# Kernel tuning notes

Measured on AMD Instinct MI355X. Metric: run time of the kernel, lower is better.

## Reference

```python
import jax, jax.numpy as jnp
import numpy as np

BULK, TOWER, E8D = 2048, 512, 8
NUM_LEVELS = 8  # training_levels
LN_EPS = 1e-6
RMS_EPS = 1e-6


def _layernorm(x, g, b, eps=LN_EPS):
    mu = jnp.mean(x, axis=-1, keepdims=True)
    var = jnp.mean((x - mu) ** 2, axis=-1, keepdims=True)
    return (x - mu) * jax.lax.rsqrt(var + eps) * g + b


def _rmsnorm(x, scale, eps=RMS_EPS):
    rms = jnp.sqrt(jnp.mean(x ** 2, axis=-1, keepdims=True) + eps)
    return x / rms * scale


def _nearest_d8(x):
    # Nearest point in D8 (integer vectors with even coordinate sum).
    f = jnp.round(x)
    err = x - f
    parity_odd = jnp.mod(jnp.sum(f, axis=-1), 2.0) != 0
    idx = jnp.argmax(jnp.abs(err), axis=-1)
    oh = jax.nn.one_hot(idx, E8D, dtype=x.dtype)
    worst_err = jnp.take_along_axis(err, idx[..., None], axis=-1)
    adj = jnp.where(worst_err >= 0, 1.0, -1.0)
    f_fix = f + oh * adj  # flip rounding of worst coordinate to restore even parity
    return jnp.where(parity_odd[..., None], f_fix, f)


def _nearest_e8(x):
    # E8 = D8 U (D8 + 1/2); pick the closer candidate.
    a = _nearest_d8(x)
    b = _nearest_d8(x - 0.5) + 0.5
    da = jnp.sum((x - a) ** 2, axis=-1)
    db = jnp.sum((x - b) ** 2, axis=-1)
    return jnp.where((da <= db)[..., None], a, b)


def _residual_e8_quantize(x, num_levels=NUM_LEVELS):
    # Residual VQ: per-level nearest E8 lattice point, subtract, accumulate.
    r = x
    q = jnp.zeros_like(x)
    for _ in range(num_levels):
        ql = _nearest_e8(r)
        q = q + ql
        r = r - ql
    return q


def setup_inputs() -> dict:
    key = jax.random.key(0)
    ks = jax.random.split(key, 8)
    B, S = 8, 2048
    s_bt = 1.0 / np.sqrt(BULK)
    s_t = 1.0 / np.sqrt(TOWER)
    s_e = 1.0 / np.sqrt(E8D)
    return {
        'x': jax.random.normal(ks[0], (B, S, BULK), dtype=jnp.float32),
        'W_bt': jax.random.uniform(ks[1], (BULK, TOWER), jnp.float32, -s_bt, s_bt),
        'b_bt': jnp.zeros((TOWER,), jnp.float32),
        'ln_et_g': jnp.ones((TOWER,), jnp.float32),
        'ln_et_b': jnp.zeros((TOWER,), jnp.float32),
        'W_t8': jax.random.uniform(ks[2], (TOWER, E8D), jnp.float32, -s_t, s_t),
        'b_t8': jnp.zeros((E8D,), jnp.float32),
        'rms_g': jnp.ones((E8D,), jnp.float32),
        'W_8t': jax.random.uniform(ks[3], (E8D, TOWER), jnp.float32, -s_e, s_e),
        'b_8t': jnp.zeros((TOWER,), jnp.float32),
        'ln_dt_g': jnp.ones((TOWER,), jnp.float32),
        'ln_dt_b': jnp.zeros((TOWER,), jnp.float32),
        'W_tb': jax.random.uniform(ks[4], (TOWER, BULK), jnp.float32, -s_t, s_t),
        'b_tb': jnp.zeros((BULK,), jnp.float32),
        'ln_db_g': jnp.ones((BULK,), jnp.float32),
        'ln_db_b': jnp.zeros((BULK,), jnp.float32),
    }


def reference(x, W_bt, b_bt, ln_et_g, ln_et_b, W_t8, b_t8, rms_g,
              W_8t, b_8t, ln_dt_g, ln_dt_b, W_tb, b_tb, ln_db_g, ln_db_b):
    B, S, D = x.shape
    h = x.reshape(B * S, D)
    # encode: bulk -> tower -> 8D continuous
    tower = _layernorm(h @ W_bt + b_bt, ln_et_g, ln_et_b)
    e8 = _rmsnorm(tower @ W_t8 + b_t8, rms_g)
    # residual E8 lattice quantization with straight-through estimator
    q = _residual_e8_quantize(e8, NUM_LEVELS)
    e8_q = e8 + jax.lax.stop_gradient(q - e8)
    # decode: 8D -> tower -> bulk
    t2 = _layernorm(e8_q @ W_8t + b_8t, ln_dt_g, ln_dt_b)
    out = _layernorm(t2 @ W_tb + b_tb, ln_db_g, ln_db_b)
    return out.reshape(B, S, D)
```

## Files before the change

### kernel.cpp

```cpp
#include <hip/hip_runtime.h>

#define BULK 2048
#define TOWER 512
#define E8D 8
#define NROWS 16384
#define LO_SCALE 2048.0f
#define LO_INV (1.0f / 2048.0f)

typedef _Float16 f16x8 __attribute__((ext_vector_type(8)));
typedef float f32x4 __attribute__((ext_vector_type(4)));

#define GLOAD(g, l)                                                        \
    __builtin_amdgcn_global_load_lds(                                      \
        (const __attribute__((address_space(1))) void*)(g),                \
        (__attribute__((address_space(3))) void*)(l), 16, 0, 0)

__global__ void k_conv_transpose(const float* __restrict__ in, int K, int N,
                                 _Float16* __restrict__ out_hi,
                                 _Float16* __restrict__ out_lo) {
    __shared__ float tile[32][33];
    int tx = threadIdx.x & 31, ty = threadIdx.x >> 5;
    int k0 = blockIdx.x * 32, n0 = blockIdx.y * 32;
#pragma unroll
    for (int i = 0; i < 32; i += 8)
        tile[ty + i][tx] = in[(size_t)(k0 + ty + i) * N + (n0 + tx)];
    __syncthreads();
#pragma unroll
    for (int i = 0; i < 32; i += 8) {
        int n = n0 + ty + i, k = k0 + tx;
        float v = tile[tx][ty + i];
        _Float16 h = (_Float16)v;
        _Float16 l = (_Float16)((v - (float)h) * LO_SCALE);
        out_hi[(size_t)n * K + k] = h;
        out_lo[(size_t)n * K + k] = l;
    }
}

template <bool A_FP32>
__global__ __launch_bounds__(256, 2) void k_gemm_split(
    const float* __restrict__ Af, const _Float16* __restrict__ Ah,
    const _Float16* __restrict__ Al, const _Float16* __restrict__ Bh,
    const _Float16* __restrict__ Bl, float* __restrict__ C, int K, int N) {
    __shared__ _Float16 lds[2][4][128][32];
    const int t = threadIdx.x;
    const int m0 = blockIdx.x * 128, n0 = blockIdx.y * 128;
    const int wid = t >> 6, lane = t & 63;
    const int wr = wid >> 1, wc = wid & 1;
    const int lr = lane & 15, kg = lane >> 4;

    f32x4 acc1[4][4] = {};
    f32x4 acc2[4][4] = {};

    const int sr = t >> 1, sc = (t & 1) * 16;
    const float* aptr = A_FP32 ? (Af + (size_t)(m0 + sr) * K + sc) : nullptr;
    float areg[16];

    const int c0 = wid * 2;
    const _Float16* bhp =
        Bh + (size_t)(n0 + c0 * 16 + (lane >> 2)) * K + (lane & 3) * 8;
    const _Float16* blp =
        Bl + (size_t)(n0 + c0 * 16 + (lane >> 2)) * K + (lane & 3) * 8;

    const _Float16* gop = (wid == 0) ? Ah : (wid == 1) ? Al : (wid == 2) ? Bh : Bl;
    const int r0 = ((wid < 2) ? m0 : n0) + (lane >> 2);
    const _Float16* gp = A_FP32 ? nullptr : (gop + (size_t)r0 * K + (lane & 3) * 8);

    auto loadA = [&](int k0) {
        const float* p = aptr + k0;
        *(float4*)&areg[0] = *(const float4*)(p);
        *(float4*)&areg[4] = *(const float4*)(p + 4);
        *(float4*)&areg[8] = *(const float4*)(p + 8);
        *(float4*)&areg[12] = *(const float4*)(p + 12);
    };
    auto stageB = [&](int k0, int bb) {
        GLOAD(bhp + k0, &lds[bb][2][c0 * 16][0]);
        GLOAD(bhp + k0 + (size_t)16 * K, &lds[bb][2][c0 * 16 + 16][0]);
        GLOAD(blp + k0, &lds[bb][3][c0 * 16][0]);
        GLOAD(blp + k0 + (size_t)16 * K, &lds[bb][3][c0 * 16 + 16][0]);
    };
    auto writeA = [&](int bb) {
        f16x8 hv0, hv1, lv0, lv1;
#pragma unroll
        for (int e = 0; e < 8; ++e) {
            float va = areg[e], vb = areg[8 + e];
            _Float16 ha = (_Float16)va, hb = (_Float16)vb;
            hv0[e] = ha;
            hv1[e] = hb;
            lv0[e] = (_Float16)((va - (float)ha) * LO_SCALE);
            lv1[e] = (_Float16)((vb - (float)hb) * LO_SCALE);
        }
        *(f16x8*)&lds[bb][0][sr][sc] = hv0;
        *(f16x8*)&lds[bb][0][sr][sc + 8] = hv1;
        *(f16x8*)&lds[bb][1][sr][sc] = lv0;
        *(f16x8*)&lds[bb][1][sr][sc + 8] = lv1;
    };
    auto stageAll = [&](int k0, int bb) {
#pragma unroll
        for (int j = 0; j < 8; ++j)
            GLOAD(gp + k0 + (size_t)(j * 16) * K, &lds[bb][wid][j * 16][0]);
    };

    if constexpr (A_FP32) {
        loadA(0);
        stageB(0, 0);
        writeA(0);
    } else {
        stageAll(0, 0);
    }
    __syncthreads();

    const int nk = K / 32;
    for (int kt = 0; kt < nk; ++kt) {
        const int b = kt & 1;
        if (kt + 1 < nk) {
            if constexpr (A_FP32) {
                loadA((kt + 1) * 32);
                stageB((kt + 1) * 32, b ^ 1);
            } else {
                stageAll((kt + 1) * 32, b ^ 1);
            }
        }

        f16x8 a_h[4], a_l[4], b_h[4], b_l[4];
#pragma unroll
        for (int m = 0; m < 4; ++m) {
            int r = wr * 64 + m * 16 + lr;
            a_h[m] = *(const f16x8*)&lds[b][0][r][kg * 8];
            a_l[m] = *(const f16x8*)&lds[b][1][r][kg * 8];
        }
#pragma unroll
        for (int n = 0; n < 4; ++n) {
            int r = wc * 64 + n * 16 + lr;
            b_h[n] = *(const f16x8*)&lds[b][2][r][kg * 8];
            b_l[n] = *(const f16x8*)&lds[b][3][r][kg * 8];
        }
#pragma unroll
        for (int m = 0; m < 4; ++m)
#pragma unroll
            for (int n = 0; n < 4; ++n) {
                acc1[m][n] = __builtin_amdgcn_mfma_f32_16x16x32_f16(
                    a_h[m], b_h[n], acc1[m][n], 0, 0, 0);
                acc2[m][n] = __builtin_amdgcn_mfma_f32_16x16x32_f16(
                    a_h[m], b_l[n], acc2[m][n], 0, 0, 0);
                acc2[m][n] = __builtin_amdgcn_mfma_f32_16x16x32_f16(
                    a_l[m], b_h[n], acc2[m][n], 0, 0, 0);
            }

        if constexpr (A_FP32) {
            if (kt + 1 < nk) writeA(b ^ 1);
        }
        __syncthreads();
    }

#pragma unroll
    for (int m = 0; m < 4; ++m)
#pragma unroll
        for (int n = 0; n < 4; ++n)
#pragma unroll
            for (int i = 0; i < 4; ++i) {
                int row = m0 + wr * 64 + m * 16 + kg * 4 + i;
                int col = n0 + wc * 64 + n * 16 + lr;
                C[(size_t)row * N + col] = acc1[m][n][i] + acc2[m][n][i] * LO_INV;
            }
}

__device__ inline void nearest_d8(const float* x, float* f) {
    float s = 0.f;
#pragma unroll
    for (int j = 0; j < 8; ++j) {
        f[j] = rintf(x[j]);
        s += f[j];
    }
    float besta = -1.f, beste = 0.f;
    int bidx = 0;
#pragma unroll
    for (int j = 0; j < 8; ++j) {
        float e = x[j] - f[j];
        float a = fabsf(e);
        if (a > besta) { besta = a; beste = e; bidx = j; }
    }
    if (fmodf(s, 2.0f) != 0.0f) {
        float adj = (beste >= 0.f) ? 1.f : -1.f;
#pragma unroll
        for (int j = 0; j < 8; ++j) f[j] += (j == bidx) ? adj : 0.f;
    }
}

__device__ inline void nearest_e8(const float* x, float* out) {
    float fa[8], xs[8], fb[8];
    nearest_d8(x, fa);
#pragma unroll
    for (int j = 0; j < 8; ++j) xs[j] = x[j] - 0.5f;
    nearest_d8(xs, fb);
#pragma unroll
    for (int j = 0; j < 8; ++j) fb[j] += 0.5f;
    float da = 0.f, db = 0.f;
#pragma unroll
    for (int j = 0; j < 8; ++j) {
        float ea = x[j] - fa[j], eb = x[j] - fb[j];
        da += ea * ea;
        db += eb * eb;
    }
    bool pa = (da <= db);
#pragma unroll
    for (int j = 0; j < 8; ++j) out[j] = pa ? fa[j] : fb[j];
}

__device__ inline float wred64(float v) {
#pragma unroll
    for (int off = 1; off < 64; off <<= 1) v += __shfl_xor(v, off, 64);
    return v;
}

__global__ __launch_bounds__(256) void k_rows(
    const float* __restrict__ pre1, const float* __restrict__ b_bt,
    const float* __restrict__ g_et, const float* __restrict__ be_et,
    const float* __restrict__ W_t8, const float* __restrict__ b_t8,
    const float* __restrict__ rms_g, const float* __restrict__ W_8t,
    const float* __restrict__ b_8t, const float* __restrict__ g_dt,
    const float* __restrict__ b_dt, _Float16* __restrict__ t2h,
    _Float16* __restrict__ t2l) {
    int wid = threadIdx.x >> 6, lane = threadIdx.x & 63;
    int row = blockIdx.x * 4 + wid;
    int cb = lane * 8;

    const float* src = pre1 + (size_t)row * TOWER + cb;
    float v[8];
    *(float4*)&v[0] = *(const float4*)(src);
    *(float4*)&v[4] = *(const float4*)(src + 4);
#pragma unroll
    for (int i = 0; i < 8; ++i) v[i] += b_bt[cb + i];

    float s = 0.f;
#pragma unroll
    for (int i = 0; i < 8; ++i) s += v[i];
    s = wred64(s);
    float mu = s * (1.f / 512.f);
    float ss = 0.f;
#pragma unroll
    for (int i = 0; i < 8; ++i) { float d = v[i] - mu; ss += d * d; }
    ss = wred64(ss);
    float inv = 1.f / sqrtf(ss * (1.f / 512.f) + 1e-6f);
    float tw[8];
#pragma unroll
    for (int i = 0; i < 8; ++i)
        tw[i] = (v[i] - mu) * inv * g_et[cb + i] + be_et[cb + i];

    float p[8] = {0.f, 0.f, 0.f, 0.f, 0.f, 0.f, 0.f, 0.f};
#pragma unroll
    for (int i = 0; i < 8; ++i) {
        const float* wr_ = W_t8 + (size_t)(cb + i) * 8;
#pragma unroll
        for (int j = 0; j < 8; ++j) p[j] += tw[i] * wr_[j];
    }
#pragma unroll
    for (int j = 0; j < 8; ++j) p[j] = wred64(p[j]);

    float e8[8];
    float ms = 0.f;
#pragma unroll
    for (int j = 0; j < 8; ++j) {
        e8[j] = p[j] + b_t8[j];
        ms += e8[j] * e8[j];
    }
    float rms = sqrtf(ms * (1.f / 8.f) + 1e-6f);
#pragma unroll
    for (int j = 0; j < 8; ++j) e8[j] = e8[j] / rms * rms_g[j];

    float q[8] = {0.f, 0.f, 0.f, 0.f, 0.f, 0.f, 0.f, 0.f};
    float r[8];
#pragma unroll
    for (int j = 0; j < 8; ++j) r[j] = e8[j];
#pragma unroll
    for (int lvl = 0; lvl < 8; ++lvl) {
        float ql[8];
        nearest_e8(r, ql);
#pragma unroll
        for (int j = 0; j < 8; ++j) { q[j] += ql[j]; r[j] -= ql[j]; }
    }

    float o[8];
#pragma unroll
    for (int i = 0; i < 8; ++i) {
        int c = cb + i;
        float acc = b_8t[c];
#pragma unroll
        for (int j = 0; j < 8; ++j) acc += q[j] * W_8t[(size_t)j * TOWER + c];
        o[i] = acc;
    }
    float s2 = 0.f;
#pragma unroll
    for (int i = 0; i < 8; ++i) s2 += o[i];
    s2 = wred64(s2);
    float mu2 = s2 * (1.f / 512.f);
    float ss2 = 0.f;
#pragma unroll
    for (int i = 0; i < 8; ++i) { float d = o[i] - mu2; ss2 += d * d; }
    ss2 = wred64(ss2);
    float inv2 = 1.f / sqrtf(ss2 * (1.f / 512.f) + 1e-6f);

    f16x8 hv, lv;
#pragma unroll
    for (int i = 0; i < 8; ++i) {
        int c = cb + i;
        float t2v = (o[i] - mu2) * inv2 * g_dt[c] + b_dt[c];
        _Float16 h = (_Float16)t2v;
        hv[i] = h;
        lv[i] = (_Float16)((t2v - (float)h) * LO_SCALE);
    }
    *(f16x8*)(t2h + (size_t)row * TOWER + cb) = hv;
    *(f16x8*)(t2l + (size_t)row * TOWER + cb) = lv;
}

__global__ __launch_bounds__(256) void k_ln2(float* __restrict__ out,
                                             const float* __restrict__ b_tb,
                                             const float* __restrict__ g,
                                             const float* __restrict__ b) {
    __shared__ float red[4];
    int t = threadIdx.x, wid = t >> 6, lane = t & 63;
    size_t base = (size_t)blockIdx.x * BULK;
    int cb = t * 8;
    float v[8];
    *(float4*)&v[0] = *(const float4*)(out + base + cb);
    *(float4*)&v[4] = *(const float4*)(out + base + cb + 4);
#pragma unroll
    for (int i = 0; i < 8; ++i) v[i] += b_tb[cb + i];

    float s = 0.f;
#pragma unroll
    for (int i = 0; i < 8; ++i) s += v[i];
    s = wred64(s);
    if (lane == 0) red[wid] = s;
    __syncthreads();
    float tot = red[0] + red[1] + red[2] + red[3];
    float mu = tot * (1.f / 2048.f);
    __syncthreads();
    float ss = 0.f;
#pragma unroll
    for (int i = 0; i < 8; ++i) { float d = v[i] - mu; ss += d * d; }
    ss = wred64(ss);
    if (lane == 0) red[wid] = ss;
    __syncthreads();
    float vtot = red[0] + red[1] + red[2] + red[3];
    float inv = 1.f / sqrtf(vtot * (1.f / 2048.f) + 1e-6f);
#pragma unroll
    for (int i = 0; i < 8; ++i) v[i] = (v[i] - mu) * inv * g[cb + i] + b[cb + i];
    *(float4*)(out + base + cb) = *(float4*)&v[0];
    *(float4*)(out + base + cb + 4) = *(float4*)&v[4];
}

extern "C" void kernel_launch(void* const* d_in, const int* in_sizes, int n_in,
                              void* d_out, int out_size, void* d_ws,
                              size_t ws_size, hipStream_t stream) {
    const float* x     = (const float*)d_in[0];
    const float* W_bt  = (const float*)d_in[1];
    const float* b_bt  = (const float*)d_in[2];
    const float* g_et  = (const float*)d_in[3];
    const float* be_et = (const float*)d_in[4];
    const float* W_t8  = (const float*)d_in[5];
    const float* b_t8  = (const float*)d_in[6];
    const float* rms_g = (const float*)d_in[7];
    const float* W_8t  = (const float*)d_in[8];
    const float* b_8t  = (const float*)d_in[9];
    const float* g_dt  = (const float*)d_in[10];
    const float* b_dt  = (const float*)d_in[11];
    const float* W_tb  = (const float*)d_in[12];
    const float* b_tb  = (const float*)d_in[13];
    const float* g_db  = (const float*)d_in[14];
    const float* b_db  = (const float*)d_in[15];
    float* out = (float*)d_out;

    char* w = (char*)d_ws;
    _Float16* Wbt_h = (_Float16*)w; w += (size_t)BULK * TOWER * 2;
    _Float16* Wbt_l = (_Float16*)w; w += (size_t)BULK * TOWER * 2;
    _Float16* Wtb_h = (_Float16*)w; w += (size_t)TOWER * BULK * 2;
    _Float16* Wtb_l = (_Float16*)w; w += (size_t)TOWER * BULK * 2;
    _Float16* t2h   = (_Float16*)w; w += (size_t)NROWS * TOWER * 2;
    _Float16* t2l   = (_Float16*)w; w += (size_t)NROWS * TOWER * 2;
    float* pre1 = out;

    k_conv_transpose<<<dim3(BULK / 32, TOWER / 32), 256, 0, stream>>>(
        W_bt, BULK, TOWER, Wbt_h, Wbt_l);
    k_conv_transpose<<<dim3(TOWER / 32, BULK / 32), 256, 0, stream>>>(
        W_tb, TOWER, BULK, Wtb_h, Wtb_l);

    k_gemm_split<true><<<dim3(NROWS / 128, TOWER / 128), 256, 0, stream>>>(
        x, nullptr, nullptr, Wbt_h, Wbt_l, pre1, BULK, TOWER);

    k_rows<<<NROWS / 4, 256, 0, stream>>>(pre1, b_bt, g_et, be_et, W_t8, b_t8,
                                          rms_g, W_8t, b_8t, g_dt, b_dt, t2h,
                                          t2l);

    k_gemm_split<false><<<dim3(NROWS / 128, BULK / 128), 256, 0, stream>>>(
        nullptr, t2h, t2l, Wtb_h, Wtb_l, out, TOWER, BULK);

    k_ln2<<<NROWS, 256, 0, stream>>>(out, b_tb, g_db, b_db);
}
```

Before: 545.0 us.

## Drop split-fp16 low part in decode GEMM and split quantization into separate kernel

The second GEMM (tower->bulk) now uses plain fp16 operands with a single MFMA per tile instead of the three-MFMA hi/lo split, which halves its LDS traffic and cuts its matrix work by about two thirds. The residual E8 quantization, which previously ran redundantly on all 64 lanes of each wave, is moved into its own kernel that runs one thread per row. Extra launches and small intermediate buffers are added. Precision of the decode projection drops to fp16 inputs, which the final layernorm may or may not tolerate.

```diff
diff --git a/kernel.cpp b/kernel.cpp
--- a/kernel.cpp
+++ b/kernel.cpp
@@ -15,6 +15,7 @@
         (const __attribute__((address_space(1))) void*)(g),                \
         (__attribute__((address_space(3))) void*)(l), 16, 0, 0)
 
+template <bool LO>
 __global__ void k_conv_transpose(const float* __restrict__ in, int K, int N,
                                  _Float16* __restrict__ out_hi,
                                  _Float16* __restrict__ out_lo) {
@@ -30,18 +31,19 @@
         int n = n0 + ty + i, k = k0 + tx;
         float v = tile[tx][ty + i];
         _Float16 h = (_Float16)v;
-        _Float16 l = (_Float16)((v - (float)h) * LO_SCALE);
         out_hi[(size_t)n * K + k] = h;
-        out_lo[(size_t)n * K + k] = l;
-    }
-}
-
-template <bool A_FP32>
+        if constexpr (LO)
+            out_lo[(size_t)n * K + k] = (_Float16)((v - (float)h) * LO_SCALE);
+    }
+}
+
+template <int MODE>
 __global__ __launch_bounds__(256, 2) void k_gemm_split(
     const float* __restrict__ Af, const _Float16* __restrict__ Ah,
-    const _Float16* __restrict__ Al, const _Float16* __restrict__ Bh,
-    const _Float16* __restrict__ Bl, float* __restrict__ C, int K, int N) {
-    __shared__ _Float16 lds[2][4][128][32];
+    const _Float16* __restrict__ Bh, const _Float16* __restrict__ Bl,
+    float* __restrict__ C, int K, int N) {
+    constexpr int NOPS = (MODE == 0) ? 4 : 2;
+    __shared__ _Float16 lds[2][NOPS][128][32];
     const int t = threadIdx.x;
     const int m0 = blockIdx.x * 128, n0 = blockIdx.y * 128;
     const int wid = t >> 6, lane = t & 63;
@@ -52,18 +54,20 @@
     f32x4 acc2[4][4] = {};
 
     const int sr = t >> 1, sc = (t & 1) * 16;
-    const float* aptr = A_FP32 ? (Af + (size_t)(m0 + sr) * K + sc) : nullptr;
+    const float* aptr = nullptr;
+    const _Float16 *bhp = nullptr, *blp = nullptr, *gp = nullptr;
     float areg[16];
-
     const int c0 = wid * 2;
-    const _Float16* bhp =
-        Bh + (size_t)(n0 + c0 * 16 + (lane >> 2)) * K + (lane & 3) * 8;
-    const _Float16* blp =
-        Bl + (size_t)(n0 + c0 * 16 + (lane >> 2)) * K + (lane & 3) * 8;
-
-    const _Float16* gop = (wid == 0) ? Ah : (wid == 1) ? Al : (wid == 2) ? Bh : Bl;
-    const int r0 = ((wid < 2) ? m0 : n0) + (lane >> 2);
-    const _Float16* gp = A_FP32 ? nullptr : (gop + (size_t)r0 * K + (lane & 3) * 8);
+
+    if constexpr (MODE == 0) {
+        aptr = Af + (size_t)(m0 + sr) * K + sc;
+        bhp = Bh + (size_t)(n0 + c0 * 16 + (lane >> 2)) * K + (lane & 3) * 8;
+        blp = Bl + (size_t)(n0 + c0 * 16 + (lane >> 2)) * K + (lane & 3) * 8;
+    } else {
+        const _Float16* gop = (wid >> 1) ? Bh : Ah;
+        const int r0 = ((wid >> 1) ? n0 : m0) + (wid & 1) * 64 + (lane >> 2);
+        gp = gop + (size_t)r0 * K + (lane & 3) * 8;
+    }
 
     auto loadA = [&](int k0) {
         const float* p = aptr + k0;
@@ -96,11 +100,12 @@
     };
     auto stageAll = [&](int k0, int bb) {
 #pragma unroll
-        for (int j = 0; j < 8; ++j)
-            GLOAD(gp + k0 + (size_t)(j * 16) * K, &lds[bb][wid][j * 16][0]);
+        for (int j = 0; j < 4; ++j)
+            GLOAD(gp + k0 + (size_t)(j * 16) * K,
+                  &lds[bb][wid >> 1][(wid & 1) * 64 + j * 16][0]);
     };
 
-    if constexpr (A_FP32) {
+    if constexpr (MODE == 0) {
         loadA(0);
         stageB(0, 0);
         writeA(0);
@@ -113,7 +118,7 @@
     for (int kt = 0; kt < nk; ++kt) {
         const int b = kt & 1;
         if (kt + 1 < nk) {
-            if constexpr (A_FP32) {
+            if constexpr (MODE == 0) {
                 loadA((kt + 1) * 32);
                 stageB((kt + 1) * 32, b ^ 1);
             } else {
@@ -121,33 +126,50 @@
             }
         }
 
-        f16x8 a_h[4], a_l[4], b_h[4], b_l[4];
-#pragma unroll
-        for (int m = 0; m < 4; ++m) {
-            int r = wr * 64 + m * 16 + lr;
-            a_h[m] = *(const f16x8*)&lds[b][0][r][kg * 8];
-            a_l[m] = *(const f16x8*)&lds[b][1][r][kg * 8];
-        }
-#pragma unroll
-        for (int n = 0; n < 4; ++n) {
-            int r = wc * 64 + n * 16 + lr;
-            b_h[n] = *(const f16x8*)&lds[b][2][r][kg * 8];
-            b_l[n] = *(const f16x8*)&lds[b][3][r][kg * 8];
-        }
-#pragma unroll
-        for (int m = 0; m < 4; ++m)
+        if constexpr (MODE == 0) {
+            f16x8 a_h[4], a_l[4], b_h[4], b_l[4];
+#pragma unroll
+            for (int m = 0; m < 4; ++m) {
+                int r = wr * 64 + m * 16 + lr;
+                a_h[m] = *(const f16x8*)&lds[b][0][r][kg * 8];
+                a_l[m] = *(const f16x8*)&lds[b][1][r][kg * 8];
+            }
 #pragma unroll
             for (int n = 0; n < 4; ++n) {
-                acc1[m][n] = __builtin_amdgcn_mfma_f32_16x16x32_f16(
-                    a_h[m], b_h[n], acc1[m][n], 0, 0, 0);
-                acc2[m][n] = __builtin_amdgcn_mfma_f32_16x16x32_f16(
-                    a_h[m], b_l[n], acc2[m][n], 0, 0, 0);
-                acc2[m][n] = __builtin_amdgcn_mfma_f32_16x16x32_f16(
-                    a_l[m], b_h[n], acc2[m][n], 0, 0, 0);
-            }
-
-        if constexpr (A_FP32) {
+                int r = wc * 64 + n * 16 + lr;
+                b_h[n] = *(const f16x8*)&lds[b][2][r][kg * 8];
+                b_l[n] = *(const f16x8*)&lds[b][3][r][kg * 8];
+            }
+#pragma unroll
+            for (int m = 0; m < 4; ++m)
+#pragma unroll
+                for (int n = 0; n < 4; ++n) {
+                    acc1[m][n] = __builtin_amdgcn_mfma_f32_16x16x32_f16(
+                        a_h[m], b_h[n], acc1[m][n], 0, 0, 0);
+                    acc2[m][n] = __builtin_amdgcn_mfma_f32_16x16x32_f16(
+                        a_h[m], b_l[n], acc2[m][n], 0, 0, 0);
+                    acc2[m][n] = __builtin_amdgcn_mfma_f32_16x16x32_f16(
+                        a_l[m], b_h[n], acc2[m][n], 0, 0, 0);
+                }
             if (kt + 1 < nk) writeA(b ^ 1);
+        } else {
+            f16x8 a_h[4], b_h[4];
+#pragma unroll
+            for (int m = 0; m < 4; ++m) {
+                int r = wr * 64 + m * 16 + lr;
+                a_h[m] = *(const f16x8*)&lds[b][0][r][kg * 8];
+            }
+#pragma unroll
+            for (int n = 0; n < 4; ++n) {
+                int r = wc * 64 + n * 16 + lr;
+                b_h[n] = *(const f16x8*)&lds[b][1][r][kg * 8];
+            }
+#pragma unroll
+            for (int m = 0; m < 4; ++m)
+#pragma unroll
+                for (int n = 0; n < 4; ++n)
+                    acc1[m][n] = __builtin_amdgcn_mfma_f32_16x16x32_f16(
+                        a_h[m], b_h[n], acc1[m][n], 0, 0, 0);
         }
         __syncthreads();
     }
@@ -160,7 +182,9 @@
             for (int i = 0; i < 4; ++i) {
                 int row = m0 + wr * 64 + m * 16 + kg * 4 + i;
                 int col = n0 + wc * 64 + n * 16 + lr;
-                C[(size_t)row * N + col] = acc1[m][n][i] + acc2[m][n][i] * LO_INV;
+                float v = acc1[m][n][i];
+                if constexpr (MODE == 0) v += acc2[m][n][i] * LO_INV;
+                C[(size_t)row * N + col] = v;
             }
 }
 
@@ -212,14 +236,11 @@
     return v;
 }
 
-__global__ __launch_bounds__(256) void k_rows(
+__global__ __launch_bounds__(256) void k_rows_a(
     const float* __restrict__ pre1, const float* __restrict__ b_bt,
     const float* __restrict__ g_et, const float* __restrict__ be_et,
     const float* __restrict__ W_t8, const float* __restrict__ b_t8,
-    const float* __restrict__ rms_g, const float* __restrict__ W_8t,
-    const float* __restrict__ b_8t, const float* __restrict__ g_dt,
-    const float* __restrict__ b_dt, _Float16* __restrict__ t2h,
-    _Float16* __restrict__ t2l) {
+    const float* __restrict__ rms_g, float* __restrict__ e8buf) {
     int wid = threadIdx.x >> 6, lane = threadIdx.x & 63;
     int row = blockIdx.x * 4 + wid;
     int cb = lane * 8;
@@ -267,10 +288,21 @@
 #pragma unroll
     for (int j = 0; j < 8; ++j) e8[j] = e8[j] / rms * rms_g[j];
 
+    if (lane == 0) {
+        float4 f0 = {e8[0], e8[1], e8[2], e8[3]};
+        float4 f1 = {e8[4], e8[5], e8[6], e8[7]};
+        *(float4*)(e8buf + (size_t)row * 8) = f0;
+        *(float4*)(e8buf + (size_t)row * 8 + 4) = f1;
+    }
+}
+
+__global__ __launch_bounds__(256) void k_quant(const float* __restrict__ e8buf,
+                                               float* __restrict__ qbuf) {
+    int row = blockIdx.x * 256 + threadIdx.x;
+    float r[8];
+    *(float4*)&r[0] = *(const float4*)(e8buf + (size_t)row * 8);
+    *(float4*)&r[4] = *(const float4*)(e8buf + (size_t)row * 8 + 4);
     float q[8] = {0.f, 0.f, 0.f, 0.f, 0.f, 0.f, 0.f, 0.f};
-    float r[8];
-#pragma unroll
-    for (int j = 0; j < 8; ++j) r[j] = e8[j];
 #pragma unroll
     for (int lvl = 0; lvl < 8; ++lvl) {
         float ql[8];
@@ -278,6 +310,23 @@
 #pragma unroll
         for (int j = 0; j < 8; ++j) { q[j] += ql[j]; r[j] -= ql[j]; }
     }
+    float4 f0 = {q[0], q[1], q[2], q[3]};
+    float4 f1 = {q[4], q[5], q[6], q[7]};
+    *(float4*)(qbuf + (size_t)row * 8) = f0;
+    *(float4*)(qbuf + (size_t)row * 8 + 4) = f1;
+}
+
+__global__ __launch_bounds__(256) void k_rows_b(
+    const float* __restrict__ qbuf, const float* __restrict__ W_8t,
+    const float* __restrict__ b_8t, const float* __restrict__ g_dt,
+    const float* __restrict__ b_dt, _Float16* __restrict__ t2h) {
+    int wid = threadIdx.x >> 6, lane = threadIdx.x & 63;
+    int row = blockIdx.x * 4 + wid;
+    int cb = lane * 8;
+
+    float q[8];
+    *(float4*)&q[0] = *(const float4*)(qbuf + (size_t)row * 8);
+    *(float4*)&q[4] = *(const float4*)(qbuf + (size_t)row * 8 + 4);
 
     float o[8];
 #pragma unroll
@@ -299,17 +348,14 @@
     ss2 = wred64(ss2);
     float inv2 = 1.f / sqrtf(ss2 * (1.f / 512.f) + 1e-6f);
 
-    f16x8 hv, lv;
+    f16x8 hv;
 #pragma unroll
     for (int i = 0; i < 8; ++i) {
         int c = cb + i;
         float t2v = (o[i] - mu2) * inv2 * g_dt[c] + b_dt[c];
-        _Float16 h = (_Float16)t2v;
-        hv[i] = h;
-        lv[i] = (_Float16)((t2v - (float)h) * LO_SCALE);
+        hv[i] = (_Float16)t2v;
     }
     *(f16x8*)(t2h + (size_t)row * TOWER + cb) = hv;
-    *(f16x8*)(t2l + (size_t)row * TOWER + cb) = lv;
 }
 
 __global__ __launch_bounds__(256) void k_ln2(float* __restrict__ out,
@@ -374,25 +420,26 @@
     _Float16* Wbt_h = (_Float16*)w; w += (size_t)BULK * TOWER * 2;
     _Float16* Wbt_l = (_Float16*)w; w += (size_t)BULK * TOWER * 2;
     _Float16* Wtb_h = (_Float16*)w; w += (size_t)TOWER * BULK * 2;
-    _Float16* Wtb_l = (_Float16*)w; w += (size_t)TOWER * BULK * 2;
     _Float16* t2h   = (_Float16*)w; w += (size_t)NROWS * TOWER * 2;
-    _Float16* t2l   = (_Float16*)w; w += (size_t)NROWS * TOWER * 2;
+    float*    e8buf = (float*)w;    w += (size_t)NROWS * E8D * 4;
+    float*    qbuf  = (float*)w;    w += (size_t)NROWS * E8D * 4;
     float* pre1 = out;
 
-    k_conv_transpose<<<dim3(BULK / 32, TOWER / 32), 256, 0, stream>>>(
+    k_conv_transpose<true><<<dim3(BULK / 32, TOWER / 32), 256, 0, stream>>>(
         W_bt, BULK, TOWER, Wbt_h, Wbt_l);
-    k_conv_transpose<<<dim3(TOWER / 32, BULK / 32), 256, 0, stream>>>(
-        W_tb, TOWER, BULK, Wtb_h, Wtb_l);
-
-    k_gemm_split<true><<<dim3(NROWS / 128, TOWER / 128), 256, 0, stream>>>(
-        x, nullptr, nullptr, Wbt_h, Wbt_l, pre1, BULK, TOWER);
-
-    k_rows<<<NROWS / 4, 256, 0, stream>>>(pre1, b_bt, g_et, be_et, W_t8, b_t8,
-                                          rms_g, W_8t, b_8t, g_dt, b_dt, t2h,
-                                          t2l);
-
-    k_gemm_split<false><<<dim3(NROWS / 128, BULK / 128), 256, 0, stream>>>(
-        nullptr, t2h, t2l, Wtb_h, Wtb_l, out, TOWER, BULK);
+    k_conv_transpose<false><<<dim3(TOWER / 32, BULK / 32), 256, 0, stream>>>(
+        W_tb, TOWER, BULK, Wtb_h, nullptr);
+
+    k_gemm_split<0><<<dim3(NROWS / 128, TOWER / 128), 256, 0, stream>>>(
+        x, nullptr, Wbt_h, Wbt_l, pre1, BULK, TOWER);
+
+    k_rows_a<<<NROWS / 4, 256, 0, stream>>>(pre1, b_bt, g_et, be_et, W_t8,
+                                            b_t8, rms_g, e8buf);
+    k_quant<<<NROWS / 256, 256, 0, stream>>>(e8buf, qbuf);
+    k_rows_b<<<NROWS / 4, 256, 0, stream>>>(qbuf, W_8t, b_8t, g_dt, b_dt, t2h);
+
+    k_gemm_split<1><<<dim3(NROWS / 128, BULK / 128), 256, 0, stream>>>(
+        nullptr, t2h, Wtb_h, nullptr, out, TOWER, BULK);
 
     k_ln2<<<NROWS, 256, 0, stream>>>(out, b_tb, g_db, b_db);
 }
```

Result: faster. 469.4 us (-13.9%).
